# Optimization experiments

Measured on AMD Instinct MI355X. Metric: run time of the kernel, lower is better.

Reference implementation:

```python
import jax, jax.numpy as jnp
import numpy as np

EPS = 1e-8  # F.cosine_similarity eps
K = 2       # prompt_length


def setup_inputs() -> dict:
    key = jax.random.key(0)
    k1, k2, k3, k4 = jax.random.split(key, 4)
    B, DIM, NP, D = 32, 64, 4, 1024   # P: [batch, dim, N_p, D]; D == V (rows of stored table)
    E, VC = 768, 32000                 # stored table [V=D, E]; f_e: E -> vocab_dim=VC
    P = jax.random.normal(k1, (B, DIM, NP, D), dtype=jnp.float32)
    we_stored = jax.random.normal(k2, (D, E), dtype=jnp.float32) * 0.02
    fe_w = jax.random.normal(k3, (VC, E), dtype=jnp.float32) * 0.02
    fe_b = jax.random.normal(k4, (VC,), dtype=jnp.float32) * 0.02
    return {"P": P, "we_stored": we_stored, "fe_w": fe_w, "fe_b": fe_b}


def reference(P, we_stored, fe_w, fe_b):
    # word_embeddings = f_e(stored).t()  ->  [vocab_dim, V] == [VC, D]
    T = (we_stored @ fe_w.T + fe_b).T            # [VC, D]
    B, DIM, NP, D = P.shape
    # Cosine sim of each tiled embedding row (repeated N_p times) vs flattened P_i:
    #   dot(tiled_w, P_flat) = w . sum_j P[..., j, :]
    #   ||tiled_w|| = sqrt(N_p) * ||w||
    s = P.sum(axis=2)                                             # [B, DIM, D]
    w_norm = jnp.maximum(jnp.sqrt(jnp.float32(NP)) * jnp.linalg.norm(T, axis=1), EPS)   # [VC]
    p_norm = jnp.maximum(jnp.linalg.norm(P.reshape(B, DIM, -1), axis=-1), EPS)          # [B, DIM]
    scores = jnp.einsum('bdk,vk->bdv', s, T) / (w_norm[None, None, :] * p_norm[..., None])  # [B, DIM, VC]
    values, indices = jax.lax.top_k(scores, K)                    # [B, DIM, K]
    e_k = T[indices]                                              # [B, DIM, K, D]
    Z = jnp.concatenate([e_k, P], axis=2)                         # [B, DIM, NP+K, D]
    return Z, values
```

## Files before the change

kernel.cpp:

```cpp
#include <hip/hip_runtime.h>
#include <hip/hip_bf16.h>
#include <math.h>

#define B_    32
#define DIM_  64
#define NP_   4
#define D_    1024
#define E_    768
#define VC_   32000
#define R_    2048
#define KTOP  2
#define EPS_  1e-8f
#define NCB   250
#define NCAND 8

#define T_OFF    ((size_t)0)
#define S_OFF    (T_OFF + (size_t)VC_ * D_)
#define INVW_OFF (S_OFF + (size_t)R_ * D_)
#define INVP_OFF (INVW_OFF + VC_)
#define WSQ_OFF  (INVP_OFF + R_)
#define PV_OFF   (WSQ_OFF + VC_)
#define PI_OFF   (PV_OFF + (size_t)R_ * NCB * 2)
#define SB_OFF   (PI_OFF + (size_t)R_ * NCB * 2)
#define TB_OFF   (SB_OFF + (size_t)R_ * D_ / 2)
#define WH_OFF   (TB_OFF + (size_t)VC_ * D_ / 2)
#define WL_OFF   (WH_OFF + (size_t)D_ * E_ / 2)
#define CAND_OFF (WL_OFF + (size_t)D_ * E_ / 2)
#define TIDX_OFF (CAND_OFF + (size_t)R_ * NCAND)
#define AH_OFF   (TIDX_OFF + (size_t)R_ * 2)
#define AL_OFF   (AH_OFF + (size_t)VC_ * E_ / 2)

#define NEG_INF (-3.4e38f)

typedef __bf16 bf16x8 __attribute__((ext_vector_type(8)));
typedef unsigned short u16x8 __attribute__((ext_vector_type(8)));
typedef float  f32x4  __attribute__((ext_vector_type(4)));

__device__ __forceinline__ void async_ld16(const void* gptr, void* lptr) {
    __builtin_amdgcn_global_load_lds(
        (const __attribute__((address_space(1))) void*)(uintptr_t)gptr,
        (__attribute__((address_space(3))) void*)(unsigned)(uintptr_t)lptr,
        16, 0, 0);
}

__device__ __forceinline__ bool better(float v, int i, float bv, int bi) {
    return (v > bv) || (v == bv && i < bi);
}

__global__ __launch_bounds__(256) void k_zero(float* __restrict__ wsq) {
    int i = blockIdx.x * 256 + threadIdx.x;
    if (i < VC_) wsq[i] = 0.f;
}

__global__ __launch_bounds__(256) void k_split(const float* __restrict__ x,
                                               unsigned short* __restrict__ hi,
                                               unsigned short* __restrict__ lo) {
    int i = (blockIdx.x * 256 + threadIdx.x) * 4;
    float4 v = *(const float4*)(x + i);
    ushort4 h, l;
    __bf16 b;
    b = (__bf16)v.x; h.x = __builtin_bit_cast(unsigned short, b); l.x = __builtin_bit_cast(unsigned short, (__bf16)(v.x - (float)b));
    b = (__bf16)v.y; h.y = __builtin_bit_cast(unsigned short, b); l.y = __builtin_bit_cast(unsigned short, (__bf16)(v.y - (float)b));
    b = (__bf16)v.z; h.z = __builtin_bit_cast(unsigned short, b); l.z = __builtin_bit_cast(unsigned short, (__bf16)(v.z - (float)b));
    b = (__bf16)v.w; h.w = __builtin_bit_cast(unsigned short, b); l.w = __builtin_bit_cast(unsigned short, (__bf16)(v.w - (float)b));
    *(ushort4*)(hi + i) = h;
    *(ushort4*)(lo + i) = l;
}

__global__ __launch_bounds__(256) void k_sum_pnorm(const float* __restrict__ P,
                                                   float* __restrict__ s,
                                                   unsigned short* __restrict__ sb,
                                                   float* __restrict__ invp) {
    int r = blockIdx.x;
    int t = threadIdx.x;
    const float* base = P + (size_t)r * NP_ * D_;
    float4 acc = make_float4(0.f, 0.f, 0.f, 0.f);
    float sq = 0.f;
#pragma unroll
    for (int np = 0; np < NP_; ++np) {
        float4 v = *(const float4*)(base + (size_t)np * D_ + t * 4);
        acc.x += v.x; acc.y += v.y; acc.z += v.z; acc.w += v.w;
        sq += v.x * v.x + v.y * v.y + v.z * v.z + v.w * v.w;
    }
    *(float4*)(s + (size_t)r * D_ + t * 4) = acc;
    ushort4 o;
    __bf16 b;
    b = (__bf16)acc.x; o.x = __builtin_bit_cast(unsigned short, b);
    b = (__bf16)acc.y; o.y = __builtin_bit_cast(unsigned short, b);
    b = (__bf16)acc.z; o.z = __builtin_bit_cast(unsigned short, b);
    b = (__bf16)acc.w; o.w = __builtin_bit_cast(unsigned short, b);
    *(ushort4*)(sb + (size_t)r * D_ + t * 4) = o;

    __shared__ float red[256];
    red[t] = sq;
    __syncthreads();
    for (int off = 128; off > 0; off >>= 1) {
        if (t < off) red[t] += red[t + off];
        __syncthreads();
    }
    if (t == 0) invp[r] = 1.0f / fmaxf(sqrtf(red[0]), EPS_);
}

__global__ __launch_bounds__(256) void k_gemm_T_mfma(const unsigned short* __restrict__ Ahg,
                                                     const unsigned short* __restrict__ Alg,
                                                     const unsigned short* __restrict__ Bhg,
                                                     const unsigned short* __restrict__ Blg,
                                                     const float* __restrict__ bias,
                                                     float* __restrict__ T,
                                                     unsigned short* __restrict__ Tb,
                                                     float* __restrict__ wsq) {
    __shared__ __align__(16) unsigned short Ash[2][128 * 32];
    __shared__ __align__(16) unsigned short Asl[2][128 * 32];
    __shared__ __align__(16) unsigned short Bsh[2][128 * 32];
    __shared__ __align__(16) unsigned short Bsl[2][128 * 32];

    int tid = threadIdx.x;
    int wid = tid >> 6, lane = tid & 63;
    int quad = lane >> 4, l15 = lane & 15;
    int id  = blockIdx.x;
    int swz = (id & 7) * 250 + (id >> 3);
    int v0 = (swz >> 3) * 128;
    int d0 = (swz & 7) * 128;
    int vband = (wid & 1) * 64, nband = (wid >> 1) * 64;

    f32x4 acc[4][4];
#pragma unroll
    for (int i = 0; i < 4; ++i)
#pragma unroll
        for (int j = 0; j < 4; ++j) acc[i][j] = f32x4{0.f, 0.f, 0.f, 0.f};

    int r_lane = lane >> 2;
    int slot   = lane & 3;

#define STAGE_G(buf, kk)                                                           \
    {                                                                              \
_Pragma("unroll")                                                                  \
        for (int j = 0; j < 2; ++j) {                                              \
            int rowt = wid * 32 + j * 16 + r_lane;                                 \
            int ss = (slot - (rowt >> 1)) & 3;                                     \
            void* la = (void*)(Ash[buf] + (wid * 32 + j * 16) * 32);               \
            void* lb = (void*)(Asl[buf] + (wid * 32 + j * 16) * 32);               \
            void* lc = (void*)(Bsh[buf] + (wid * 32 + j * 16) * 32);               \
            void* ld = (void*)(Bsl[buf] + (wid * 32 + j * 16) * 32);               \
            async_ld16(Ahg + (size_t)(v0 + rowt) * E_ + (kk) + ss * 8, la);        \
            async_ld16(Alg + (size_t)(v0 + rowt) * E_ + (kk) + ss * 8, lb);        \
            async_ld16(Bhg + (size_t)(d0 + rowt) * E_ + (kk) + ss * 8, lc);        \
            async_ld16(Blg + (size_t)(d0 + rowt) * E_ + (kk) + ss * 8, ld);        \
        }                                                                          \
    }

    int cur = 0;
    STAGE_G(0, 0);
    __syncthreads();

    for (int k0 = 0; k0 < E_; k0 += 32) {
        if (k0 + 32 < E_) STAGE_G(cur ^ 1, k0 + 32);

        bf16x8 fah[4], fal[4], fbh[4], fbl[4];
#pragma unroll
        for (int mt = 0; mt < 4; ++mt) {
            int row = vband + mt * 16 + l15;
            int ps = (quad + (row >> 1)) & 3;
            int off = row * 32 + ps * 8;
            fah[mt] = *(const bf16x8*)(Ash[cur] + off);
            fal[mt] = *(const bf16x8*)(Asl[cur] + off);
        }
#pragma unroll
        for (int nt = 0; nt < 4; ++nt) {
            int row = nband + nt * 16 + l15;
            int ps = (quad + (row >> 1)) & 3;
            int off = row * 32 + ps * 8;
            fbh[nt] = *(const bf16x8*)(Bsh[cur] + off);
            fbl[nt] = *(const bf16x8*)(Bsl[cur] + off);
        }
#pragma unroll
        for (int mt = 0; mt < 4; ++mt)
#pragma unroll
            for (int nt = 0; nt < 4; ++nt) {
                acc[mt][nt] = __builtin_amdgcn_mfma_f32_16x16x32_bf16(fah[mt], fbh[nt], acc[mt][nt], 0, 0, 0);
                acc[mt][nt] = __builtin_amdgcn_mfma_f32_16x16x32_bf16(fal[mt], fbh[nt], acc[mt][nt], 0, 0, 0);
                acc[mt][nt] = __builtin_amdgcn_mfma_f32_16x16x32_bf16(fah[mt], fbl[nt], acc[mt][nt], 0, 0, 0);
            }

        __syncthreads();
        cur ^= 1;
    }
#undef STAGE_G

    float sq[4][4] = {};
#pragma unroll
    for (int mt = 0; mt < 4; ++mt) {
        int vbase = v0 + vband + mt * 16 + quad * 4;
        float bv[4];
#pragma unroll
        for (int rg = 0; rg < 4; ++rg) bv[rg] = bias[vbase + rg];
#pragma unroll
        for (int nt = 0; nt < 4; ++nt) {
            int d = d0 + nband + nt * 16 + l15;
#pragma unroll
            for (int rg = 0; rg < 4; ++rg) {
                float val = acc[mt][nt][rg] + bv[rg];
                T[(size_t)(vbase + rg) * D_ + d] = val;
                __bf16 vb = (__bf16)val;
                Tb[(size_t)(vbase + rg) * D_ + d] = __builtin_bit_cast(unsigned short, vb);
                sq[mt][rg] += val * val;
            }
        }
    }
#pragma unroll
    for (int mt = 0; mt < 4; ++mt)
#pragma unroll
        for (int rg = 0; rg < 4; ++rg) {
            float p = sq[mt][rg];
            p += __shfl_xor(p, 1); p += __shfl_xor(p, 2);
            p += __shfl_xor(p, 4); p += __shfl_xor(p, 8);
            if (l15 == 0) atomicAdd(&wsq[v0 + vband + mt * 16 + quad * 4 + rg], p);
        }
}

__global__ __launch_bounds__(256) void k_invw(const float* __restrict__ wsq,
                                              float* __restrict__ invw) {
    int v = blockIdx.x * 256 + threadIdx.x;
    if (v < VC_) invw[v] = 1.0f / fmaxf(2.0f * sqrtf(wsq[v]), EPS_);
}

__global__ __launch_bounds__(256) void k_scores_mfma(const unsigned short* __restrict__ Tb,
                                                     const unsigned short* __restrict__ sb,
                                                     const float* __restrict__ invw,
                                                     float* __restrict__ pval,
                                                     int* __restrict__ pidx) {
    __shared__ __align__(16) unsigned short As[2][128 * 32];
    __shared__ __align__(16) unsigned short Bs[2][128 * 32];
    __shared__ float mv[2][128][2];
    __shared__ int   mi[2][128][2];

    int tid = threadIdx.x;
    int wid = tid >> 6, lane = tid & 63;
    int quad = lane >> 4, l15 = lane & 15;
    int id   = blockIdx.x;
    int swz  = (id & 7) * 500 + (id >> 3);
    int vblk = swz >> 4;
    int rblk = swz & 15;
    int v0 = vblk * 128;
    int r0 = rblk * 128;
    int vband = (wid & 1) * 64, rband = (wid >> 1) * 64;

    f32x4 acc[4][4];
#pragma unroll
    for (int i = 0; i < 4; ++i)
#pragma unroll
        for (int j = 0; j < 4; ++j) acc[i][j] = f32x4{0.f, 0.f, 0.f, 0.f};

    int r_lane = lane >> 2;
    int slot   = lane & 3;

#define STAGE_SC(buf, kk)                                                          \
    {                                                                              \
_Pragma("unroll")                                                                  \
        for (int j = 0; j < 2; ++j) {                                              \
            int rowt = wid * 32 + j * 16 + r_lane;                                 \
            int ss = (slot - (rowt >> 1)) & 3;                                     \
            async_ld16(Tb + (size_t)(v0 + rowt) * D_ + (kk) + ss * 8,              \
                       (void*)(As[buf] + (wid * 32 + j * 16) * 32));               \
            async_ld16(sb + (size_t)(r0 + rowt) * D_ + (kk) + ss * 8,              \
                       (void*)(Bs[buf] + (wid * 32 + j * 16) * 32));               \
        }                                                                          \
    }

    int cur = 0;
    STAGE_SC(0, 0);
    __syncthreads();

    for (int k0 = 0; k0 < D_; k0 += 32) {
        if (k0 + 32 < D_) STAGE_SC(cur ^ 1, k0 + 32);

        bf16x8 af[4], bfr[4];
#pragma unroll
        for (int mt = 0; mt < 4; ++mt) {
            int row = vband + mt * 16 + l15;
            int ps = (quad + (row >> 1)) & 3;
            af[mt] = *(const bf16x8*)(As[cur] + row * 32 + ps * 8);
        }
#pragma unroll
        for (int nt = 0; nt < 4; ++nt) {
            int row = rband + nt * 16 + l15;
            int ps = (quad + (row >> 1)) & 3;
            bfr[nt] = *(const bf16x8*)(Bs[cur] + row * 32 + ps * 8);
        }
#pragma unroll
        for (int mt = 0; mt < 4; ++mt)
#pragma unroll
            for (int nt = 0; nt < 4; ++nt)
                acc[mt][nt] = __builtin_amdgcn_mfma_f32_16x16x32_bf16(af[mt], bfr[nt], acc[mt][nt], 0, 0, 0);

        __syncthreads();
        cur ^= 1;
    }
#undef STAGE_SC

    float iw[4][4];
#pragma unroll
    for (int mt = 0; mt < 4; ++mt)
#pragma unroll
        for (int rg = 0; rg < 4; ++rg)
            iw[mt][rg] = invw[v0 + vband + mt * 16 + quad * 4 + rg];

#pragma unroll
    for (int nt = 0; nt < 4; ++nt) {
        float b1 = NEG_INF, b2 = NEG_INF;
        int i1 = 0x7fffffff, i2 = 0x7fffffff;
#pragma unroll
        for (int mt = 0; mt < 4; ++mt)
#pragma unroll
            for (int rg = 0; rg < 4; ++rg) {
                float val = acc[mt][nt][rg] * iw[mt][rg];
                int v = v0 + vband + mt * 16 + quad * 4 + rg;
                if (better(val, v, b1, i1)) { b2 = b1; i2 = i1; b1 = val; i1 = v; }
                else if (better(val, v, b2, i2)) { b2 = val; i2 = v; }
            }
#pragma unroll
        for (int off = 16; off <= 32; off <<= 1) {
            float o1 = __shfl_xor(b1, off), o2 = __shfl_xor(b2, off);
            int  oi1 = __shfl_xor(i1, off), oi2 = __shfl_xor(i2, off);
            if (better(o1, oi1, b1, i1)) {
                if (better(b1, i1, o2, oi2)) { b2 = b1; i2 = i1; } else { b2 = o2; i2 = oi2; }
                b1 = o1; i1 = oi1;
            } else if (better(o1, oi1, b2, i2)) { b2 = o1; i2 = oi1; }
        }
        if (quad == 0) {
            int rl = rband + nt * 16 + l15;
            mv[wid & 1][rl][0] = b1; mi[wid & 1][rl][0] = i1;
            mv[wid & 1][rl][1] = b2; mi[wid & 1][rl][1] = i2;
        }
    }
    __syncthreads();
    if (tid < 128) {
        float b1 = mv[0][tid][0], b2 = mv[0][tid][1];
        int   i1 = mi[0][tid][0], i2 = mi[0][tid][1];
#pragma unroll
        for (int sl = 0; sl < 2; ++sl) {
            float o = mv[1][tid][sl]; int oi = mi[1][tid][sl];
            if (better(o, oi, b1, i1)) { b2 = b1; i2 = i1; b1 = o; i1 = oi; }
            else if (better(o, oi, b2, i2)) { b2 = o; i2 = oi; }
        }
        size_t off = ((size_t)(r0 + tid) * NCB + vblk) * 2;
        pval[off] = b1;     pidx[off] = i1;
        pval[off + 1] = b2; pidx[off + 1] = i2;
    }
}

__global__ __launch_bounds__(256) void k_topk8(const float* __restrict__ pval,
                                               const int* __restrict__ pidx,
                                               int* __restrict__ cands) {
    int r = blockIdx.x, t = threadIdx.x;
    __shared__ float v[512];
    __shared__ int  id[512];
    for (int c = t; c < 512; c += 256) {
        if (c < NCB * 2) { v[c] = pval[(size_t)r * NCB * 2 + c]; id[c] = pidx[(size_t)r * NCB * 2 + c]; }
        else             { v[c] = NEG_INF; id[c] = 0x7fffffff; }
    }
    __syncthreads();
    if (t == 0) {
        float bv[NCAND]; int bi[NCAND];
#pragma unroll
        for (int j = 0; j < NCAND; ++j) { bv[j] = NEG_INF; bi[j] = 0x7fffffff; }
        for (int c = 0; c < NCB * 2; ++c) {
            float x = v[c]; int xi = id[c];
            if (better(x, xi, bv[NCAND - 1], bi[NCAND - 1])) {
                int j = NCAND - 1;
                while (j > 0 && better(x, xi, bv[j - 1], bi[j - 1])) {
                    bv[j] = bv[j - 1]; bi[j] = bi[j - 1]; --j;
                }
                bv[j] = x; bi[j] = xi;
            }
        }
#pragma unroll
        for (int j = 0; j < NCAND; ++j) cands[r * NCAND + j] = bi[j];
    }
}

__global__ __launch_bounds__(256) void k_rescore(const float* __restrict__ s,
                                                 const float* __restrict__ T,
                                                 const int* __restrict__ cands,
                                                 const float* __restrict__ invw,
                                                 const float* __restrict__ invp,
                                                 float* __restrict__ outv,
                                                 int* __restrict__ tidx) {
    int r = blockIdx.x, t = threadIdx.x;
    int cg = t >> 5, l32 = t & 31;
    int c = cands[r * NCAND + cg];
    const float* Trow = T + (size_t)c * D_;
    const float* srow = s + (size_t)r * D_;
    float p = 0.f;
#pragma unroll
    for (int j = 0; j < 8; ++j) {
        int e = (j * 32 + l32) * 4;
        float4 a = *(const float4*)(srow + e);
        float4 b = *(const float4*)(Trow + e);
        p += a.x * b.x + a.y * b.y + a.z * b.z + a.w * b.w;
    }
#pragma unroll
    for (int off = 16; off >= 1; off >>= 1) p += __shfl_xor(p, off);
    __shared__ float sc[NCAND];
    if (l32 == 0) sc[cg] = p;
    __syncthreads();
    if (t == 0) {
        float ip = invp[r];
        float b1 = NEG_INF, b2 = NEG_INF;
        int i1 = 0x7fffffff, i2 = 0x7fffffff;
#pragma unroll
        for (int j = 0; j < NCAND; ++j) {
            int ci = cands[r * NCAND + j];
            float val = sc[j] * invw[ci] * ip;
            if (better(val, ci, b1, i1)) { b2 = b1; i2 = i1; b1 = val; i1 = ci; }
            else if (better(val, ci, b2, i2)) { b2 = val; i2 = ci; }
        }
        outv[(size_t)r * 2 + 0] = b1;
        outv[(size_t)r * 2 + 1] = b2;
        tidx[r * 2 + 0] = i1;
        tidx[r * 2 + 1] = i2;
    }
}

__global__ __launch_bounds__(256) void k_writeZ(const float* __restrict__ P,
                                                const float* __restrict__ T,
                                                const int* __restrict__ tidx,
                                                float* __restrict__ out) {
    int blk = blockIdx.x;
    int r = blk / 6, j = blk - r * 6;
    const float* src;
    if (j < KTOP) src = T + (size_t)tidx[r * 2 + j] * D_;
    else          src = P + ((size_t)r * NP_ + (j - KTOP)) * D_;
    float4 v = *(const float4*)(src + threadIdx.x * 4);
    *(float4*)(out + ((size_t)r * 6 + j) * D_ + threadIdx.x * 4) = v;
}

extern "C" void kernel_launch(void* const* d_in, const int* in_sizes, int n_in,
                              void* d_out, int out_size, void* d_ws, size_t ws_size,
                              hipStream_t stream) {
    const float* P   = (const float*)d_in[0];
    const float* we  = (const float*)d_in[1];
    const float* few = (const float*)d_in[2];
    const float* feb = (const float*)d_in[3];
    float* out = (float*)d_out;
    float* ws  = (float*)d_ws;

    float* T    = ws + T_OFF;
    float* s    = ws + S_OFF;
    float* invw = ws + INVW_OFF;
    float* invp = ws + INVP_OFF;
    float* wsq  = ws + WSQ_OFF;
    float* pval = ws + PV_OFF;
    int*   pidx = (int*)(ws + PI_OFF);
    unsigned short* sb  = (unsigned short*)(ws + SB_OFF);
    unsigned short* Tb  = (unsigned short*)(ws + TB_OFF);
    unsigned short* weh = (unsigned short*)(ws + WH_OFF);
    unsigned short* wel = (unsigned short*)(ws + WL_OFF);
    int*   cands = (int*)(ws + CAND_OFF);
    int*   tidx  = (int*)(ws + TIDX_OFF);
    unsigned short* fewh = (unsigned short*)(ws + AH_OFF);
    unsigned short* fewl = (unsigned short*)(ws + AL_OFF);
    float* outv = out + (size_t)R_ * 6 * D_;

    k_zero<<<(VC_ + 255) / 256, 256, 0, stream>>>(wsq);
    k_split<<<(D_ * E_) / 1024, 256, 0, stream>>>(we, weh, wel);
    k_split<<<((size_t)VC_ * E_) / 1024, 256, 0, stream>>>(few, fewh, fewl);
    k_sum_pnorm<<<R_, 256, 0, stream>>>(P, s, sb, invp);
    k_gemm_T_mfma<<<2000, 256, 0, stream>>>(fewh, fewl, weh, wel, feb, T, Tb, wsq);
    k_invw<<<(VC_ + 255) / 256, 256, 0, stream>>>(wsq, invw);
    k_scores_mfma<<<4000, 256, 0, stream>>>(Tb, sb, invw, pval, pidx);
    k_topk8<<<R_, 256, 0, stream>>>(pval, pidx, cands);
    k_rescore<<<R_, 256, 0, stream>>>(s, T, cands, invw, invp, outv, tidx);
    k_writeZ<<<R_ * 6, 256, 0, stream>>>(P, T, tidx, out);
}
```

Before: 684.6 us.

## Enlarge scores GEMM tile to 256x256 with 4-stage async pipeline

The scores kernel moves from 128x128 tiles with 4 waves and double buffering to 256x256 tiles with 8 waves, a 4-deep LDS ring buffer, explicit vmcnt waits and raw barriers, and setprio around the MFMA block. The per-block shared-memory merge of the two wave halves is removed. Each wave instead writes its own top-2 partial directly, and each 128-row v-half maps to its own candidate slot, keeping NCB at 250. The aim is to raise arithmetic intensity and hide global-load latency. In exchange it uses 128KB of LDS and more accumulator registers, which lowers occupancy.

New measurement: 661.5 us. 1.03x faster.

```diff
diff --git a/kernel.cpp b/kernel.cpp
--- a/kernel.cpp
+++ b/kernel.cpp
@@ -224,30 +224,28 @@
     if (v < VC_) invw[v] = 1.0f / fmaxf(2.0f * sqrtf(wsq[v]), EPS_);
 }
 
-__global__ __launch_bounds__(256) void k_scores_mfma(const unsigned short* __restrict__ Tb,
+__global__ __launch_bounds__(512) void k_scores_mfma(const unsigned short* __restrict__ Tb,
                                                      const unsigned short* __restrict__ sb,
                                                      const float* __restrict__ invw,
                                                      float* __restrict__ pval,
                                                      int* __restrict__ pidx) {
-    __shared__ __align__(16) unsigned short As[2][128 * 32];
-    __shared__ __align__(16) unsigned short Bs[2][128 * 32];
-    __shared__ float mv[2][128][2];
-    __shared__ int   mi[2][128][2];
+    __shared__ __align__(16) unsigned short As[4][256 * 32];
+    __shared__ __align__(16) unsigned short Bs[4][256 * 32];
 
     int tid = threadIdx.x;
     int wid = tid >> 6, lane = tid & 63;
     int quad = lane >> 4, l15 = lane & 15;
+    int wm = wid >> 2, wn = wid & 3;
     int id   = blockIdx.x;
-    int swz  = (id & 7) * 500 + (id >> 3);
-    int vblk = swz >> 4;
-    int rblk = swz & 15;
-    int v0 = vblk * 128;
-    int r0 = rblk * 128;
-    int vband = (wid & 1) * 64, rband = (wid >> 1) * 64;
-
-    f32x4 acc[4][4];
-#pragma unroll
-    for (int i = 0; i < 4; ++i)
+    int swz  = (id & 7) * 125 + (id >> 3);
+    int vblk = swz >> 3;
+    int rblk = swz & 7;
+    int v0 = vblk * 256;
+    int r0 = rblk * 256;
+
+    f32x4 acc[8][4];
+#pragma unroll
+    for (int i = 0; i < 8; ++i)
 #pragma unroll
         for (int j = 0; j < 4; ++j) acc[i][j] = f32x4{0.f, 0.f, 0.f, 0.f};
 
@@ -258,63 +256,71 @@
     {                                                                              \
 _Pragma("unroll")                                                                  \
         for (int j = 0; j < 2; ++j) {                                              \
-            int rowt = wid * 32 + j * 16 + r_lane;                                 \
+            int rowt = j * 128 + wid * 16 + r_lane;                                \
             int ss = (slot - (rowt >> 1)) & 3;                                     \
             async_ld16(Tb + (size_t)(v0 + rowt) * D_ + (kk) + ss * 8,              \
-                       (void*)(As[buf] + (wid * 32 + j * 16) * 32));               \
+                       (void*)(As[buf] + (j * 128 + wid * 16) * 32));              \
             async_ld16(sb + (size_t)(r0 + rowt) * D_ + (kk) + ss * 8,              \
-                       (void*)(Bs[buf] + (wid * 32 + j * 16) * 32));               \
+                       (void*)(Bs[buf] + (j * 128 + wid * 16) * 32));              \
         }                                                                          \
     }
 
-    int cur = 0;
     STAGE_SC(0, 0);
-    __syncthreads();
-
-    for (int k0 = 0; k0 < D_; k0 += 32) {
-        if (k0 + 32 < D_) STAGE_SC(cur ^ 1, k0 + 32);
-
-        bf16x8 af[4], bfr[4];
-#pragma unroll
-        for (int mt = 0; mt < 4; ++mt) {
-            int row = vband + mt * 16 + l15;
-            int ps = (quad + (row >> 1)) & 3;
-            af[mt] = *(const bf16x8*)(As[cur] + row * 32 + ps * 8);
-        }
+    STAGE_SC(1, 32);
+    STAGE_SC(2, 64);
+
+    const int NT = D_ / 32;
+    for (int kt = 0; kt < NT; ++kt) {
+        int cur = kt & 3;
+        int kn  = (kt + 3 < NT) ? (kt + 3) * 32 : kt * 32;
+        STAGE_SC((kt + 3) & 3, kn);
+
+        asm volatile("s_waitcnt vmcnt(12)" ::: "memory");
+        __builtin_amdgcn_s_barrier();
+        asm volatile("" ::: "memory");
+
+        bf16x8 bfr[4];
 #pragma unroll
         for (int nt = 0; nt < 4; ++nt) {
-            int row = rband + nt * 16 + l15;
+            int row = wn * 64 + nt * 16 + l15;
             int ps = (quad + (row >> 1)) & 3;
             bfr[nt] = *(const bf16x8*)(Bs[cur] + row * 32 + ps * 8);
         }
-#pragma unroll
-        for (int mt = 0; mt < 4; ++mt)
+        __builtin_amdgcn_s_setprio(1);
+#pragma unroll
+        for (int mt = 0; mt < 8; ++mt) {
+            int row = wm * 128 + mt * 16 + l15;
+            int ps = (quad + (row >> 1)) & 3;
+            bf16x8 af = *(const bf16x8*)(As[cur] + row * 32 + ps * 8);
 #pragma unroll
             for (int nt = 0; nt < 4; ++nt)
-                acc[mt][nt] = __builtin_amdgcn_mfma_f32_16x16x32_bf16(af[mt], bfr[nt], acc[mt][nt], 0, 0, 0);
-
-        __syncthreads();
-        cur ^= 1;
+                acc[mt][nt] = __builtin_amdgcn_mfma_f32_16x16x32_bf16(af, bfr[nt], acc[mt][nt], 0, 0, 0);
+        }
+        __builtin_amdgcn_s_setprio(0);
+
+        __builtin_amdgcn_sched_barrier(0);
+        __builtin_amdgcn_s_barrier();
+        asm volatile("" ::: "memory");
     }
 #undef STAGE_SC
 
-    float iw[4][4];
-#pragma unroll
-    for (int mt = 0; mt < 4; ++mt)
+    float iw[8][4];
+#pragma unroll
+    for (int mt = 0; mt < 8; ++mt)
 #pragma unroll
         for (int rg = 0; rg < 4; ++rg)
-            iw[mt][rg] = invw[v0 + vband + mt * 16 + quad * 4 + rg];
+            iw[mt][rg] = invw[v0 + wm * 128 + mt * 16 + quad * 4 + rg];
 
 #pragma unroll
     for (int nt = 0; nt < 4; ++nt) {
         float b1 = NEG_INF, b2 = NEG_INF;
         int i1 = 0x7fffffff, i2 = 0x7fffffff;
 #pragma unroll
-        for (int mt = 0; mt < 4; ++mt)
+        for (int mt = 0; mt < 8; ++mt)
 #pragma unroll
             for (int rg = 0; rg < 4; ++rg) {
                 float val = acc[mt][nt][rg] * iw[mt][rg];
-                int v = v0 + vband + mt * 16 + quad * 4 + rg;
+                int v = v0 + wm * 128 + mt * 16 + quad * 4 + rg;
                 if (better(val, v, b1, i1)) { b2 = b1; i2 = i1; b1 = val; i1 = v; }
                 else if (better(val, v, b2, i2)) { b2 = val; i2 = v; }
             }
@@ -328,24 +334,11 @@
             } else if (better(o1, oi1, b2, i2)) { b2 = o1; i2 = oi1; }
         }
         if (quad == 0) {
-            int rl = rband + nt * 16 + l15;
-            mv[wid & 1][rl][0] = b1; mi[wid & 1][rl][0] = i1;
-            mv[wid & 1][rl][1] = b2; mi[wid & 1][rl][1] = i2;
-        }
-    }
-    __syncthreads();
-    if (tid < 128) {
-        float b1 = mv[0][tid][0], b2 = mv[0][tid][1];
-        int   i1 = mi[0][tid][0], i2 = mi[0][tid][1];
-#pragma unroll
-        for (int sl = 0; sl < 2; ++sl) {
-            float o = mv[1][tid][sl]; int oi = mi[1][tid][sl];
-            if (better(o, oi, b1, i1)) { b2 = b1; i2 = i1; b1 = o; i1 = oi; }
-            else if (better(o, oi, b2, i2)) { b2 = o; i2 = oi; }
-        }
-        size_t off = ((size_t)(r0 + tid) * NCB + vblk) * 2;
-        pval[off] = b1;     pidx[off] = i1;
-        pval[off + 1] = b2; pidx[off + 1] = i2;
+            int rl = wn * 64 + nt * 16 + l15;
+            size_t off = ((size_t)(r0 + rl) * NCB + vblk * 2 + wm) * 2;
+            pval[off] = b1;     pidx[off] = i1;
+            pval[off + 1] = b2; pidx[off + 1] = i2;
+        }
     }
 }
 
@@ -468,7 +461,7 @@
     k_sum_pnorm<<<R_, 256, 0, stream>>>(P, s, sb, invp);
     k_gemm_T_mfma<<<2000, 256, 0, stream>>>(fewh, fewl, weh, wel, feb, T, Tb, wsq);
     k_invw<<<(VC_ + 255) / 256, 256, 0, stream>>>(wsq, invw);
-    k_scores_mfma<<<4000, 256, 0, stream>>>(Tb, sb, invw, pval, pidx);
+    k_scores_mfma<<<1000, 512, 0, stream>>>(Tb, sb, invw, pval, pidx);
     k_topk8<<<R_, 256, 0, stream>>>(pval, pidx, cands);
     k_rescore<<<R_, 256, 0, stream>>>(s, T, cands, invw, invp, outv, tidx);
     k_writeZ<<<R_ * 6, 256, 0, stream>>>(P, T, tidx, out);
```
